# Optimization experiments

Measured on AMD Instinct MI355X. Metric: run time of the kernel, lower is better.

The kernel has to match this reference:

```python
import jax, jax.numpy as jnp
import numpy as np

N_NODES = 100000
N_EDGES = 3200000
F_IN = 128
H = 32
C = 8


def _graph_conv(x, src, dst, ew, W_rel, b_rel, W_root):
    # PyG GraphConv: sum-aggregate edge_weight * x[src] into dst, then
    # lin_rel(agg) + lin_root(x). lin_root has no bias.
    msg = x[src] * ew[:, None]                                  # [E, F]
    agg = jax.ops.segment_sum(msg, dst, num_segments=N_NODES)   # [N, F]
    return agg @ W_rel.T + b_rel + x @ W_root.T


def setup_inputs() -> dict:
    key = jax.random.key(0)
    ks = jax.random.split(key, 12)
    x = jax.random.normal(ks[0], (N_NODES, F_IN), dtype=jnp.float32)
    edge_index = jax.random.randint(ks[1], (2, N_EDGES), 0, N_NODES, dtype=jnp.int32)
    edge_weights = jax.random.uniform(ks[2], (N_EDGES,), dtype=jnp.float32)
    s = lambda fan_in: 1.0 / np.sqrt(fan_in)
    W1_rel = jax.random.uniform(ks[3], (H, F_IN), minval=-s(F_IN), maxval=s(F_IN), dtype=jnp.float32)
    b1 = jax.random.uniform(ks[4], (H,), minval=-s(F_IN), maxval=s(F_IN), dtype=jnp.float32)
    W1_root = jax.random.uniform(ks[5], (H, F_IN), minval=-s(F_IN), maxval=s(F_IN), dtype=jnp.float32)
    W2_rel = jax.random.uniform(ks[6], (H, H), minval=-s(H), maxval=s(H), dtype=jnp.float32)
    b2 = jax.random.uniform(ks[7], (H,), minval=-s(H), maxval=s(H), dtype=jnp.float32)
    W2_root = jax.random.uniform(ks[8], (H, H), minval=-s(H), maxval=s(H), dtype=jnp.float32)
    W3_rel = jax.random.uniform(ks[9], (C, H), minval=-s(H), maxval=s(H), dtype=jnp.float32)
    b3 = jax.random.uniform(ks[10], (C,), minval=-s(H), maxval=s(H), dtype=jnp.float32)
    W3_root = jax.random.uniform(ks[11], (C, H), minval=-s(H), maxval=s(H), dtype=jnp.float32)
    return {"x": x, "edge_index": edge_index, "edge_weights": edge_weights,
            "W1_rel": W1_rel, "b1": b1, "W1_root": W1_root,
            "W2_rel": W2_rel, "b2": b2, "W2_root": W2_root,
            "W3_rel": W3_rel, "b3": b3, "W3_root": W3_root}


def reference(x, edge_index, edge_weights,
              W1_rel, b1, W1_root, W2_rel, b2, W2_root, W3_rel, b3, W3_root):
    src, dst = edge_index[0], edge_index[1]
    h = _graph_conv(x, src, dst, edge_weights, W1_rel, b1, W1_root)
    h = jax.nn.leaky_relu(h, negative_slope=0.01)
    # dropout is identity in eval mode
    h = _graph_conv(h, src, dst, edge_weights, W2_rel, b2, W2_root)
    h = jax.nn.leaky_relu(h, negative_slope=0.01)
    out = _graph_conv(h, src, dst, edge_weights, W3_rel, b3, W3_root)
    return out
```

## Files before the change

### kernel.cpp

```cpp
#include <hip/hip_runtime.h>

#define NN 100000
#define NE 3200000
#define NE4 (NE / 4)
#define FIN 128
#define HD 32
#define CD 8
#define NPB 256
#define NBUCK ((NN + NPB - 1) / NPB)
#define CHUNK_B 8192

typedef unsigned int uint;

__device__ __forceinline__ float lrelu(float v) { return v > 0.f ? v : 0.01f * v; }
__device__ __forceinline__ uint bf16rne(float x) {
    uint u = __float_as_uint(x);
    return (u + 0x7FFFu + ((u >> 16) & 1u)) >> 16;
}
__device__ __forceinline__ uint pack2(float a, float b) {
    return bf16rne(a) | (bf16rne(b) << 16);
}
__device__ __forceinline__ float lo16(uint v) { return __uint_as_float(v << 16); }
__device__ __forceinline__ float hi16(uint v) { return __uint_as_float(v & 0xFFFF0000u); }


__global__ __launch_bounds__(256) void k_proj128(
    const float* __restrict__ x, const float* __restrict__ Wrel,
    const float* __restrict__ Wroot, const float* __restrict__ b,
    uint* __restrict__ pB, float* __restrict__ R)
{
    __shared__ float Wt[FIN][64];
    for (int idx = threadIdx.x; idx < FIN * 64; idx += 256) {
        int k = idx >> 6, j = idx & 63;
        Wt[k][j] = (j < HD) ? Wrel[j * FIN + k] : Wroot[(j - HD) * FIN + k];
    }
    __syncthreads();
    int n = blockIdx.x * 256 + threadIdx.x;
    if (n >= NN) return;

    float accP[HD], accR[HD];
#pragma unroll
    for (int j = 0; j < HD; ++j) { accP[j] = 0.f; accR[j] = 0.f; }

    const float4* x4 = (const float4*)(x + (size_t)n * FIN);
#pragma unroll 2
    for (int k4 = 0; k4 < FIN / 4; ++k4) {
        float4 xv = x4[k4];
        float xs[4] = {xv.x, xv.y, xv.z, xv.w};
#pragma unroll
        for (int kk = 0; kk < 4; ++kk) {
            float xk = xs[kk];
            int k = k4 * 4 + kk;
#pragma unroll
            for (int j = 0; j < HD; ++j) {
                accP[j] += xk * Wt[k][j];
                accR[j] += xk * Wt[k][j + HD];
            }
        }
    }
    uint4* pp = (uint4*)(pB + (size_t)n * 16);
#pragma unroll
    for (int q = 0; q < 4; ++q)
        pp[q] = make_uint4(pack2(accP[8*q+0], accP[8*q+1]), pack2(accP[8*q+2], accP[8*q+3]),
                           pack2(accP[8*q+4], accP[8*q+5]), pack2(accP[8*q+6], accP[8*q+7]));
    float4* rr = (float4*)(R + (size_t)n * HD);
#pragma unroll
    for (int q = 0; q < HD / 4; ++q)
        rr[q] = make_float4(accR[4*q+0] + b[4*q+0], accR[4*q+1] + b[4*q+1],
                            accR[4*q+2] + b[4*q+2], accR[4*q+3] + b[4*q+3]);
}


__global__ __launch_bounds__(512) void k_bhist(
    const int* __restrict__ dst, int* __restrict__ bcnt)
{
    __shared__ int lc[NBUCK];
    int t = threadIdx.x;
    for (int i = t; i < NBUCK; i += 512) lc[i] = 0;
    __syncthreads();
    const int4* dst4 = (const int4*)dst;
    for (int i4 = blockIdx.x * 512 + t; i4 < NE4; i4 += gridDim.x * 512) {
        int4 d = dst4[i4];
        atomicAdd(&lc[d.x >> 8], 1);
        atomicAdd(&lc[d.y >> 8], 1);
        atomicAdd(&lc[d.z >> 8], 1);
        atomicAdd(&lc[d.w >> 8], 1);
    }
    __syncthreads();
    for (int i = t; i < NBUCK; i += 512) {
        int c = lc[i];
        if (c) atomicAdd(&bcnt[i], c);
    }
}

__global__ __launch_bounds__(512) void k_bscan(
    const int* __restrict__ bcnt, int* __restrict__ bbase, int* __restrict__ bcur)
{
    __shared__ int s[512];
    int t = threadIdx.x;
    s[t] = (t < NBUCK) ? bcnt[t] : 0;
    __syncthreads();
    for (int off = 1; off < 512; off <<= 1) {
        int a = (t >= off) ? s[t - off] : 0;
        __syncthreads();
        s[t] += a;
        __syncthreads();
    }
    int excl = t ? s[t - 1] : 0;
    if (t < NBUCK) { bbase[t] = excl; bcur[t] = excl; }
    if (t == 0) bbase[NBUCK] = NE;
}

__global__ __launch_bounds__(512) void k_bscatter(
    const int* __restrict__ src, const int* __restrict__ dst, const float* __restrict__ ew,
    int* __restrict__ bcur, int2* __restrict__ tmp)
{
    __shared__ int lc[NBUCK];
    int t = threadIdx.x;
    for (int i = t; i < NBUCK; i += 512) lc[i] = 0;
    __syncthreads();
    const int4* dst4 = (const int4*)dst;
    const int4* src4 = (const int4*)src;
    const float4* ew4 = (const float4*)ew;
    int base4 = blockIdx.x * (CHUNK_B / 4);
#pragma unroll
    for (int k = 0; k < CHUNK_B / 4 / 512; ++k) {
        int i4 = base4 + k * 512 + t;
        if (i4 < NE4) {
            int4 d = dst4[i4];
            atomicAdd(&lc[d.x >> 8], 1);
            atomicAdd(&lc[d.y >> 8], 1);
            atomicAdd(&lc[d.z >> 8], 1);
            atomicAdd(&lc[d.w >> 8], 1);
        }
    }
    __syncthreads();
    for (int b = t; b < NBUCK; b += 512) {
        int c = lc[b];
        lc[b] = c ? atomicAdd(&bcur[b], c) : 0;
    }
    __syncthreads();
#pragma unroll
    for (int k = 0; k < CHUNK_B / 4 / 512; ++k) {
        int i4 = base4 + k * 512 + t;
        if (i4 < NE4) {
            int4 d = dst4[i4];
            int4 s = src4[i4];
            float4 w = ew4[i4];
            int pos;
            pos = atomicAdd(&lc[d.x >> 8], 1); tmp[pos] = make_int2(s.x | ((d.x & 255) << 17), __float_as_int(w.x));
            pos = atomicAdd(&lc[d.y >> 8], 1); tmp[pos] = make_int2(s.y | ((d.y & 255) << 17), __float_as_int(w.y));
            pos = atomicAdd(&lc[d.z >> 8], 1); tmp[pos] = make_int2(s.z | ((d.z & 255) << 17), __float_as_int(w.z));
            pos = atomicAdd(&lc[d.w >> 8], 1); tmp[pos] = make_int2(s.w | ((d.w & 255) << 17), __float_as_int(w.w));
        }
    }
}

__global__ __launch_bounds__(512) void k_bsort(
    const int* __restrict__ bbase, const int2* __restrict__ tmp,
    int2* __restrict__ epack, int* __restrict__ rowstart)
{
    int b = blockIdx.x, t = threadIdx.x;
    int lo = bbase[b], hi = bbase[b + 1], cnt = hi - lo;
    __shared__ int hist[NPB];
    __shared__ int sc[NPB];
    __shared__ int cur[NPB];
    if (t < NPB) hist[t] = 0;
    __syncthreads();
    for (int i = t; i < cnt; i += 512)
        atomicAdd(&hist[(tmp[lo + i].x >> 17) & 255], 1);
    __syncthreads();
    if (t < NPB) sc[t] = hist[t];
    __syncthreads();
    for (int off = 1; off < NPB; off <<= 1) {
        int a = (t < NPB && t >= off) ? sc[t - off] : 0;
        __syncthreads();
        if (t < NPB) sc[t] += a;
        __syncthreads();
    }
    if (t < NPB) {
        int excl = t ? sc[t - 1] : 0;
        int node = (b << 8) + t;
        if (node < NN) rowstart[node] = lo + excl;
        cur[t] = lo + excl;
    }
    if (b == 0 && t == 0) rowstart[NN] = NE;
    __syncthreads();
    for (int i = t; i < cnt; i += 512) {
        int2 v = tmp[lo + i];
        int l = (v.x >> 17) & 255;
        int pos = atomicAdd(&cur[l], 1);
        epack[pos] = make_int2(v.x & 0x1FFFF, v.y);
    }
}


__global__ __launch_bounds__(256) void k_gatherMid(
    const int* __restrict__ rowstart, const int2* __restrict__ epack,
    const uint* __restrict__ pB1, float* R,
    const float* __restrict__ Wrel, const float* __restrict__ Wroot,
    const float* __restrict__ b2, uint* __restrict__ pB2)
{
    __shared__ float Ws[HD][64];
    __shared__ float hS[4][HD];
    for (int idx = threadIdx.x; idx < HD * 64; idx += 256) {
        int k = idx >> 6, j = idx & 63;
        Ws[k][j] = (j < HD) ? Wrel[j * HD + k] : Wroot[(j - HD) * HD + k];
    }
    int wid = (blockIdx.x * 256 + threadIdx.x) >> 6;
    int lane = threadIdx.x & 63;
    int w = threadIdx.x >> 6;
    int q = lane >> 4, f2 = lane & 15;
    int rs = rowstart[wid], re = rowstart[wid + 1];

    float a0 = 0.f, a1 = 0.f, c0 = 0.f, c1 = 0.f, d0 = 0.f, d1 = 0.f;
    int e = rs + q;
    for (; e + 8 < re; e += 12) {
        int2 p0 = epack[e];
        int2 p1 = epack[e + 4];
        int2 p2 = epack[e + 8];
        uint v0 = pB1[((size_t)p0.x << 4) + f2];
        uint v1 = pB1[((size_t)p1.x << 4) + f2];
        uint v2 = pB1[((size_t)p2.x << 4) + f2];
        float w0 = __int_as_float(p0.y), w1 = __int_as_float(p1.y), w2 = __int_as_float(p2.y);
        a0 += lo16(v0) * w0; a1 += hi16(v0) * w0;
        c0 += lo16(v1) * w1; c1 += hi16(v1) * w1;
        d0 += lo16(v2) * w2; d1 += hi16(v2) * w2;
    }
    for (; e < re; e += 4) {
        int2 p0 = epack[e];
        uint v0 = pB1[((size_t)p0.x << 4) + f2];
        float w0 = __int_as_float(p0.y);
        a0 += lo16(v0) * w0; a1 += hi16(v0) * w0;
    }
    a0 += c0 + d0; a1 += c1 + d1;
    a0 += __shfl_xor(a0, 16); a1 += __shfl_xor(a1, 16);
    a0 += __shfl_xor(a0, 32); a1 += __shfl_xor(a1, 32);
    if (lane < 16) {
        float2 rv = *(const float2*)(R + (size_t)wid * HD + 2 * f2);
        float2 hv = make_float2(lrelu(a0 + rv.x), lrelu(a1 + rv.y));
        *(float2*)&hS[w][2 * f2] = hv;
    }
    __syncthreads();

    int j = lane;
    float acc = 0.f;
#pragma unroll 8
    for (int k = 0; k < HD; ++k) acc += hS[w][k] * Ws[k][j];
    float other = __shfl_xor(acc, 1);
    if (j < HD) {
        if (!(j & 1)) pB2[(size_t)wid * 16 + (j >> 1)] = pack2(acc, other);
    } else {
        R[(size_t)wid * HD + (j - HD)] = acc + b2[j - HD];
    }
}

__global__ __launch_bounds__(256) void k_gatherLast(
    const int* __restrict__ rowstart, const int2* __restrict__ epack,
    const uint* __restrict__ pB2, const float* __restrict__ R,
    const float* __restrict__ Wrel, const float* __restrict__ Wroot,
    const float* __restrict__ b3, uint* __restrict__ p3B, float* __restrict__ out)
{
    __shared__ float Ws[HD][16];
    __shared__ float hS[4][HD];
    for (int idx = threadIdx.x; idx < HD * 16; idx += 256) {
        int k = idx >> 4, j = idx & 15;
        Ws[k][j] = (j < CD) ? Wrel[j * HD + k] : Wroot[(j - CD) * HD + k];
    }
    int wid = (blockIdx.x * 256 + threadIdx.x) >> 6;
    int lane = threadIdx.x & 63;
    int w = threadIdx.x >> 6;
    int q = lane >> 4, f2 = lane & 15;
    int rs = rowstart[wid], re = rowstart[wid + 1];

    float a0 = 0.f, a1 = 0.f, c0 = 0.f, c1 = 0.f, d0 = 0.f, d1 = 0.f;
    int e = rs + q;
    for (; e + 8 < re; e += 12) {
        int2 p0 = epack[e];
        int2 p1 = epack[e + 4];
        int2 p2 = epack[e + 8];
        uint v0 = pB2[((size_t)p0.x << 4) + f2];
        uint v1 = pB2[((size_t)p1.x << 4) + f2];
        uint v2 = pB2[((size_t)p2.x << 4) + f2];
        float w0 = __int_as_float(p0.y), w1 = __int_as_float(p1.y), w2 = __int_as_float(p2.y);
        a0 += lo16(v0) * w0; a1 += hi16(v0) * w0;
        c0 += lo16(v1) * w1; c1 += hi16(v1) * w1;
        d0 += lo16(v2) * w2; d1 += hi16(v2) * w2;
    }
    for (; e < re; e += 4) {
        int2 p0 = epack[e];
        uint v0 = pB2[((size_t)p0.x << 4) + f2];
        float w0 = __int_as_float(p0.y);
        a0 += lo16(v0) * w0; a1 += hi16(v0) * w0;
    }
    a0 += c0 + d0; a1 += c1 + d1;
    a0 += __shfl_xor(a0, 16); a1 += __shfl_xor(a1, 16);
    a0 += __shfl_xor(a0, 32); a1 += __shfl_xor(a1, 32);
    if (lane < 16) {
        float2 rv = *(const float2*)(R + (size_t)wid * HD + 2 * f2);
        float2 hv = make_float2(lrelu(a0 + rv.x), lrelu(a1 + rv.y));
        *(float2*)&hS[w][2 * f2] = hv;
    }
    __syncthreads();

    if (lane < 16) {
        int j = lane;
        float acc = 0.f;
#pragma unroll 8
        for (int k = 0; k < HD; ++k) acc += hS[w][k] * Ws[k][j];
        float other = __shfl_xor(acc, 1);
        if (j < CD) {
            if (!(j & 1)) p3B[(size_t)wid * 4 + (j >> 1)] = pack2(acc, other);
        } else {
            out[(size_t)wid * CD + (j - CD)] = acc + b3[j - CD];
        }
    }
}

__global__ __launch_bounds__(256) void k_gather8(
    const int* __restrict__ rowstart, const int2* __restrict__ epack,
    const uint* __restrict__ p3B, float* __restrict__ out)
{
    int wid = (blockIdx.x * 256 + threadIdx.x) >> 6;
    if (wid >= NN) return;
    int lane = threadIdx.x & 63;
    int q = lane >> 2, f2 = lane & 3;
    int rs = rowstart[wid], re = rowstart[wid + 1];

    float a0 = 0.f, a1 = 0.f, b0 = 0.f, b1 = 0.f;
    int e = rs + q;
    for (; e + 16 < re; e += 32) {
        int2 p0 = epack[e];
        int2 p1 = epack[e + 16];
        uint v0 = p3B[((size_t)p0.x << 2) + f2];
        uint v1 = p3B[((size_t)p1.x << 2) + f2];
        float w0 = __int_as_float(p0.y), w1 = __int_as_float(p1.y);
        a0 += lo16(v0) * w0; a1 += hi16(v0) * w0;
        b0 += lo16(v1) * w1; b1 += hi16(v1) * w1;
    }
    for (; e < re; e += 16) {
        int2 p0 = epack[e];
        uint v0 = p3B[((size_t)p0.x << 2) + f2];
        float w0 = __int_as_float(p0.y);
        a0 += lo16(v0) * w0; a1 += hi16(v0) * w0;
    }
    a0 += b0; a1 += b1;
    a0 += __shfl_xor(a0, 4);  a1 += __shfl_xor(a1, 4);
    a0 += __shfl_xor(a0, 8);  a1 += __shfl_xor(a1, 8);
    a0 += __shfl_xor(a0, 16); a1 += __shfl_xor(a1, 16);
    a0 += __shfl_xor(a0, 32); a1 += __shfl_xor(a1, 32);
    if (lane < 4) {
        float2* o2 = (float2*)(out + (size_t)wid * CD + 2 * f2);
        float2 t = *o2;
        t.x += a0; t.y += a1;
        *o2 = t;
    }
}


extern "C" void kernel_launch(void* const* d_in, const int* in_sizes, int n_in,
                              void* d_out, int out_size, void* d_ws, size_t ws_size,
                              hipStream_t stream)
{
    const float* x      = (const float*)d_in[0];
    const int*   ei     = (const int*)d_in[1];
    const float* ew     = (const float*)d_in[2];
    const float* W1rel  = (const float*)d_in[3];
    const float* b1     = (const float*)d_in[4];
    const float* W1root = (const float*)d_in[5];
    const float* W2rel  = (const float*)d_in[6];
    const float* b2     = (const float*)d_in[7];
    const float* W2root = (const float*)d_in[8];
    const float* W3rel  = (const float*)d_in[9];
    const float* b3     = (const float*)d_in[10];
    const float* W3root = (const float*)d_in[11];
    float* out = (float*)d_out;

    const int* src = ei;
    const int* dst = ei + NE;

    char* ws = (char*)d_ws;
    int2*  epack    = (int2*)ws;   ws += (size_t)NE * sizeof(int2);
    int2*  tmp      = (int2*)ws;   ws += (size_t)NE * sizeof(int2);
    float* R        = (float*)ws;  ws += (size_t)NN * HD * 4;
    uint*  pB1      = (uint*)ws;   ws += (size_t)NN * 16 * 4;
    uint*  pB2      = (uint*)ws;   ws += (size_t)NN * 16 * 4;
    uint*  p3B      = (uint*)ws;   ws += (size_t)NN * 4 * 4;
    int*   rowstart = (int*)ws;    ws += (size_t)(NN + 1) * 4;
    int*   bcnt     = (int*)ws;    ws += (size_t)NBUCK * 4;
    int*   bbase    = (int*)ws;    ws += (size_t)(NBUCK + 1) * 4;
    int*   bcur     = (int*)ws;

    const int nodeBlocks = (NN + 255) / 256;
    const int waveBlocks = (NN + 3) / 4;
    const int scatBlocks = (NE + CHUNK_B - 1) / CHUNK_B;

    hipMemsetAsync(bcnt, 0, (size_t)NBUCK * 4, stream);
    k_bhist<<<512, 512, 0, stream>>>(dst, bcnt);
    k_bscan<<<1, 512, 0, stream>>>(bcnt, bbase, bcur);
    k_bscatter<<<scatBlocks, 512, 0, stream>>>(src, dst, ew, bcur, tmp);
    k_bsort<<<NBUCK, 512, 0, stream>>>(bbase, tmp, epack, rowstart);

    k_proj128<<<nodeBlocks, 256, 0, stream>>>(x, W1rel, W1root, b1, pB1, R);
    k_gatherMid<<<waveBlocks, 256, 0, stream>>>(rowstart, epack, pB1, R, W2rel, W2root, b2, pB2);
    k_gatherLast<<<waveBlocks, 256, 0, stream>>>(rowstart, epack, pB2, R, W3rel, W3root, b3, p3B, out);
    k_gather8<<<waveBlocks, 256, 0, stream>>>(rowstart, epack, p3B, out);
}
```

Baseline: 525.5 us.

## Locally sort scatter chunk in LDS for coalesced bucket writes; shuffle-based mid matvec

The bucket scatter kernel now ranks each chunk's edges in shared memory by bucket, builds a permutation, and writes each bucket's edges to global memory contiguously. This replaces the scattered per-edge global writes of the old version. The mid and last gather kernels drop the shared-memory staging of h and broadcast it with lane shuffles instead, and they unroll the edge loop to four independent accumulators. The changes add shared-memory use (about 56KB per scatter block) and re-read dst/src/ew in permuted order, which can lower occupancy.

```diff
diff --git a/kernel.cpp b/kernel.cpp
--- a/kernel.cpp
+++ b/kernel.cpp
@@ -11,6 +11,7 @@
 #define CHUNK_B 8192
 
 typedef unsigned int uint;
+typedef unsigned short ushort;
 
 __device__ __forceinline__ float lrelu(float v) { return v > 0.f ? v : 0.01f * v; }
 __device__ __forceinline__ uint bf16rne(float x) {
@@ -115,44 +116,49 @@
     const int* __restrict__ src, const int* __restrict__ dst, const float* __restrict__ ew,
     int* __restrict__ bcur, int2* __restrict__ tmp)
 {
-    __shared__ int lc[NBUCK];
+    __shared__ int cnt[NBUCK];
+    __shared__ int s[512];
+    __shared__ int excl[NBUCK];
+    __shared__ int goff[NBUCK];
+    __shared__ uint rk[CHUNK_B];
+    __shared__ ushort perm[CHUNK_B];
     int t = threadIdx.x;
-    for (int i = t; i < NBUCK; i += 512) lc[i] = 0;
-    __syncthreads();
-    const int4* dst4 = (const int4*)dst;
-    const int4* src4 = (const int4*)src;
-    const float4* ew4 = (const float4*)ew;
-    int base4 = blockIdx.x * (CHUNK_B / 4);
-#pragma unroll
-    for (int k = 0; k < CHUNK_B / 4 / 512; ++k) {
-        int i4 = base4 + k * 512 + t;
-        if (i4 < NE4) {
-            int4 d = dst4[i4];
-            atomicAdd(&lc[d.x >> 8], 1);
-            atomicAdd(&lc[d.y >> 8], 1);
-            atomicAdd(&lc[d.z >> 8], 1);
-            atomicAdd(&lc[d.w >> 8], 1);
-        }
-    }
-    __syncthreads();
-    for (int b = t; b < NBUCK; b += 512) {
-        int c = lc[b];
-        lc[b] = c ? atomicAdd(&bcur[b], c) : 0;
-    }
-    __syncthreads();
-#pragma unroll
-    for (int k = 0; k < CHUNK_B / 4 / 512; ++k) {
-        int i4 = base4 + k * 512 + t;
-        if (i4 < NE4) {
-            int4 d = dst4[i4];
-            int4 s = src4[i4];
-            float4 w = ew4[i4];
-            int pos;
-            pos = atomicAdd(&lc[d.x >> 8], 1); tmp[pos] = make_int2(s.x | ((d.x & 255) << 17), __float_as_int(w.x));
-            pos = atomicAdd(&lc[d.y >> 8], 1); tmp[pos] = make_int2(s.y | ((d.y & 255) << 17), __float_as_int(w.y));
-            pos = atomicAdd(&lc[d.z >> 8], 1); tmp[pos] = make_int2(s.z | ((d.z & 255) << 17), __float_as_int(w.z));
-            pos = atomicAdd(&lc[d.w >> 8], 1); tmp[pos] = make_int2(s.w | ((d.w & 255) << 17), __float_as_int(w.w));
-        }
+    int base = blockIdx.x * CHUNK_B;
+    int n = min(CHUNK_B, NE - base);
+
+    for (int i = t; i < NBUCK; i += 512) cnt[i] = 0;
+    __syncthreads();
+    for (int i = t; i < n; i += 512) {
+        int b = dst[base + i] >> 8;
+        int r = atomicAdd(&cnt[b], 1);
+        rk[i] = ((uint)b << 13) | (uint)r;
+    }
+    __syncthreads();
+    int myc = (t < NBUCK) ? cnt[t] : 0;
+    s[t] = myc;
+    __syncthreads();
+    for (int o = 1; o < 512; o <<= 1) {
+        int a = (t >= o) ? s[t - o] : 0;
+        __syncthreads();
+        s[t] += a;
+        __syncthreads();
+    }
+    if (t < NBUCK) {
+        excl[t] = s[t] - myc;
+        goff[t] = myc ? atomicAdd(&bcur[t], myc) : 0;
+    }
+    __syncthreads();
+    for (int i = t; i < n; i += 512) {
+        uint v = rk[i];
+        perm[excl[v >> 13] + (v & 8191u)] = (ushort)i;
+    }
+    __syncthreads();
+    for (int j = t; j < n; j += 512) {
+        int i = (int)perm[j];
+        int d = dst[base + i];
+        int b = d >> 8;
+        tmp[goff[b] + (j - excl[b])] =
+            make_int2(src[base + i] | ((d & 255) << 17), __float_as_int(ew[base + i]));
     }
 }
 
@@ -195,37 +201,43 @@
 }
 
 
-__global__ __launch_bounds__(256) void k_gatherMid(
+__global__ __launch_bounds__(256) void k_gMid(
     const int* __restrict__ rowstart, const int2* __restrict__ epack,
     const uint* __restrict__ pB1, float* R,
     const float* __restrict__ Wrel, const float* __restrict__ Wroot,
     const float* __restrict__ b2, uint* __restrict__ pB2)
 {
     __shared__ float Ws[HD][64];
-    __shared__ float hS[4][HD];
     for (int idx = threadIdx.x; idx < HD * 64; idx += 256) {
         int k = idx >> 6, j = idx & 63;
         Ws[k][j] = (j < HD) ? Wrel[j * HD + k] : Wroot[(j - HD) * HD + k];
     }
+    __syncthreads();
+
     int wid = (blockIdx.x * 256 + threadIdx.x) >> 6;
+    if (wid >= NN) return;
     int lane = threadIdx.x & 63;
-    int w = threadIdx.x >> 6;
     int q = lane >> 4, f2 = lane & 15;
     int rs = rowstart[wid], re = rowstart[wid + 1];
 
-    float a0 = 0.f, a1 = 0.f, c0 = 0.f, c1 = 0.f, d0 = 0.f, d1 = 0.f;
+    float a0 = 0.f, a1 = 0.f, b0 = 0.f, b1 = 0.f;
+    float c0 = 0.f, c1 = 0.f, d0 = 0.f, d1 = 0.f;
     int e = rs + q;
-    for (; e + 8 < re; e += 12) {
+    for (; e + 12 < re; e += 16) {
         int2 p0 = epack[e];
         int2 p1 = epack[e + 4];
         int2 p2 = epack[e + 8];
+        int2 p3 = epack[e + 12];
         uint v0 = pB1[((size_t)p0.x << 4) + f2];
         uint v1 = pB1[((size_t)p1.x << 4) + f2];
         uint v2 = pB1[((size_t)p2.x << 4) + f2];
-        float w0 = __int_as_float(p0.y), w1 = __int_as_float(p1.y), w2 = __int_as_float(p2.y);
-        a0 += lo16(v0) * w0; a1 += hi16(v0) * w0;
-        c0 += lo16(v1) * w1; c1 += hi16(v1) * w1;
-        d0 += lo16(v2) * w2; d1 += hi16(v2) * w2;
+        uint v3 = pB1[((size_t)p3.x << 4) + f2];
+        float w0 = __int_as_float(p0.y), w1 = __int_as_float(p1.y);
+        float w2 = __int_as_float(p2.y), w3 = __int_as_float(p3.y);
+        a0 += lo16(v0) * w0; a1 += hi16(v0) * w0;
+        b0 += lo16(v1) * w1; b1 += hi16(v1) * w1;
+        c0 += lo16(v2) * w2; c1 += hi16(v2) * w2;
+        d0 += lo16(v3) * w3; d1 += hi16(v3) * w3;
     }
     for (; e < re; e += 4) {
         int2 p0 = epack[e];
@@ -233,20 +245,22 @@
         float w0 = __int_as_float(p0.y);
         a0 += lo16(v0) * w0; a1 += hi16(v0) * w0;
     }
-    a0 += c0 + d0; a1 += c1 + d1;
+    a0 += b0 + c0 + d0; a1 += b1 + c1 + d1;
     a0 += __shfl_xor(a0, 16); a1 += __shfl_xor(a1, 16);
     a0 += __shfl_xor(a0, 32); a1 += __shfl_xor(a1, 32);
-    if (lane < 16) {
-        float2 rv = *(const float2*)(R + (size_t)wid * HD + 2 * f2);
-        float2 hv = make_float2(lrelu(a0 + rv.x), lrelu(a1 + rv.y));
-        *(float2*)&hS[w][2 * f2] = hv;
-    }
-    __syncthreads();
+
+    float2 rv = *(const float2*)(R + (size_t)wid * HD + 2 * f2);
+    float h0 = lrelu(a0 + rv.x);
+    float h1 = lrelu(a1 + rv.y);
 
     int j = lane;
     float acc = 0.f;
-#pragma unroll 8
-    for (int k = 0; k < HD; ++k) acc += hS[w][k] * Ws[k][j];
+#pragma unroll
+    for (int k = 0; k < HD; k += 2) {
+        float ha = __shfl(h0, k >> 1);
+        float hb = __shfl(h1, k >> 1);
+        acc += ha * Ws[k][j] + hb * Ws[k + 1][j];
+    }
     float other = __shfl_xor(acc, 1);
     if (j < HD) {
         if (!(j & 1)) pB2[(size_t)wid * 16 + (j >> 1)] = pack2(acc, other);
@@ -255,37 +269,43 @@
     }
 }
 
-__global__ __launch_bounds__(256) void k_gatherLast(
+__global__ __launch_bounds__(256) void k_gLast(
     const int* __restrict__ rowstart, const int2* __restrict__ epack,
     const uint* __restrict__ pB2, const float* __restrict__ R,
     const float* __restrict__ Wrel, const float* __restrict__ Wroot,
     const float* __restrict__ b3, uint* __restrict__ p3B, float* __restrict__ out)
 {
     __shared__ float Ws[HD][16];
-    __shared__ float hS[4][HD];
     for (int idx = threadIdx.x; idx < HD * 16; idx += 256) {
         int k = idx >> 4, j = idx & 15;
         Ws[k][j] = (j < CD) ? Wrel[j * HD + k] : Wroot[(j - CD) * HD + k];
     }
+    __syncthreads();
+
     int wid = (blockIdx.x * 256 + threadIdx.x) >> 6;
+    if (wid >= NN) return;
     int lane = threadIdx.x & 63;
-    int w = threadIdx.x >> 6;
     int q = lane >> 4, f2 = lane & 15;
     int rs = rowstart[wid], re = rowstart[wid + 1];
 
-    float a0 = 0.f, a1 = 0.f, c0 = 0.f, c1 = 0.f, d0 = 0.f, d1 = 0.f;
+    float a0 = 0.f, a1 = 0.f, b0 = 0.f, b1 = 0.f;
+    float c0 = 0.f, c1 = 0.f, d0 = 0.f, d1 = 0.f;
     int e = rs + q;
-    for (; e + 8 < re; e += 12) {
+    for (; e + 12 < re; e += 16) {
         int2 p0 = epack[e];
         int2 p1 = epack[e + 4];
         int2 p2 = epack[e + 8];
+        int2 p3 = epack[e + 12];
         uint v0 = pB2[((size_t)p0.x << 4) + f2];
         uint v1 = pB2[((size_t)p1.x << 4) + f2];
         uint v2 = pB2[((size_t)p2.x << 4) + f2];
-        float w0 = __int_as_float(p0.y), w1 = __int_as_float(p1.y), w2 = __int_as_float(p2.y);
-        a0 += lo16(v0) * w0; a1 += hi16(v0) * w0;
-        c0 += lo16(v1) * w1; c1 += hi16(v1) * w1;
-        d0 += lo16(v2) * w2; d1 += hi16(v2) * w2;
+        uint v3 = pB2[((size_t)p3.x << 4) + f2];
+        float w0 = __int_as_float(p0.y), w1 = __int_as_float(p1.y);
+        float w2 = __int_as_float(p2.y), w3 = __int_as_float(p3.y);
+        a0 += lo16(v0) * w0; a1 += hi16(v0) * w0;
+        b0 += lo16(v1) * w1; b1 += hi16(v1) * w1;
+        c0 += lo16(v2) * w2; c1 += hi16(v2) * w2;
+        d0 += lo16(v3) * w3; d1 += hi16(v3) * w3;
     }
     for (; e < re; e += 4) {
         int2 p0 = epack[e];
@@ -293,27 +313,27 @@
         float w0 = __int_as_float(p0.y);
         a0 += lo16(v0) * w0; a1 += hi16(v0) * w0;
     }
-    a0 += c0 + d0; a1 += c1 + d1;
+    a0 += b0 + c0 + d0; a1 += b1 + c1 + d1;
     a0 += __shfl_xor(a0, 16); a1 += __shfl_xor(a1, 16);
     a0 += __shfl_xor(a0, 32); a1 += __shfl_xor(a1, 32);
-    if (lane < 16) {
-        float2 rv = *(const float2*)(R + (size_t)wid * HD + 2 * f2);
-        float2 hv = make_float2(lrelu(a0 + rv.x), lrelu(a1 + rv.y));
-        *(float2*)&hS[w][2 * f2] = hv;
-    }
-    __syncthreads();
-
-    if (lane < 16) {
-        int j = lane;
-        float acc = 0.f;
-#pragma unroll 8
-        for (int k = 0; k < HD; ++k) acc += hS[w][k] * Ws[k][j];
-        float other = __shfl_xor(acc, 1);
-        if (j < CD) {
-            if (!(j & 1)) p3B[(size_t)wid * 4 + (j >> 1)] = pack2(acc, other);
-        } else {
-            out[(size_t)wid * CD + (j - CD)] = acc + b3[j - CD];
-        }
+
+    float2 rv = *(const float2*)(R + (size_t)wid * HD + 2 * f2);
+    float h0 = lrelu(a0 + rv.x);
+    float h1 = lrelu(a1 + rv.y);
+
+    int j = lane;
+    float acc = 0.f;
+#pragma unroll
+    for (int k = 0; k < HD; k += 2) {
+        float ha = __shfl(h0, k >> 1);
+        float hb = __shfl(h1, k >> 1);
+        if (j < 16) acc += ha * Ws[k][j] + hb * Ws[k + 1][j];
+    }
+    float other = __shfl_xor(acc, 1);
+    if (j < CD) {
+        if (!(j & 1)) p3B[(size_t)wid * 4 + (j >> 1)] = pack2(acc, other);
+    } else if (j < 16) {
+        out[(size_t)wid * CD + (j - CD)] = acc + b3[j - CD];
     }
 }
 
@@ -402,7 +422,7 @@
     k_bsort<<<NBUCK, 512, 0, stream>>>(bbase, tmp, epack, rowstart);
 
     k_proj128<<<nodeBlocks, 256, 0, stream>>>(x, W1rel, W1root, b1, pB1, R);
-    k_gatherMid<<<waveBlocks, 256, 0, stream>>>(rowstart, epack, pB1, R, W2rel, W2root, b2, pB2);
-    k_gatherLast<<<waveBlocks, 256, 0, stream>>>(rowstart, epack, pB2, R, W3rel, W3root, b3, p3B, out);
+    k_gMid<<<waveBlocks, 256, 0, stream>>>(rowstart, epack, pB1, R, W2rel, W2root, b2, pB2);
+    k_gLast<<<waveBlocks, 256, 0, stream>>>(rowstart, epack, pB2, R, W3rel, W3root, b3, p3B, out);
     k_gather8<<<waveBlocks, 256, 0, stream>>>(rowstart, epack, p3B, out);
 }
```

Measured after the change: 547.1 us. 4.1% more time.
